# Optimization experiments

Measured on AMD Instinct MI355X. Metric: run time of the kernel, lower is better.

## Reference

```python
import jax, jax.numpy as jnp
import numpy as np

N_NODES = 2048
N_PAIRS = 65536
D = 512
P = 16


def setup_inputs() -> dict:
    key = jax.random.key(0)
    ks = jax.random.split(key, 9)
    scale = 1.0 / np.sqrt(D)
    obj_feats = jax.random.normal(ks[0], (N_NODES, D), dtype=jnp.float32)
    union_feats = jax.random.normal(ks[1], (N_PAIRS, D), dtype=jnp.float32)
    pair_idxs = jax.random.randint(ks[2], (N_PAIRS, 2), 0, N_NODES, dtype=jnp.int64)
    ws_w = jax.random.uniform(ks[3], (D, D), jnp.float32, -scale, scale)
    ws_b = jax.random.uniform(ks[4], (D,), jnp.float32, -scale, scale)
    wo_w = jax.random.uniform(ks[5], (D, D), jnp.float32, -scale, scale)
    wo_b = jax.random.uniform(ks[6], (D,), jnp.float32, -scale, scale)
    w_w = jax.random.uniform(ks[7], (P, D), jnp.float32, -scale, scale)
    w_b = jax.random.uniform(ks[8], (P,), jnp.float32, -scale, scale)
    return {
        'obj_feats': obj_feats, 'union_feats': union_feats, 'pair_idxs': pair_idxs,
        'ws_w': ws_w, 'ws_b': ws_b, 'wo_w': wo_w, 'wo_b': wo_b, 'w_w': w_w, 'w_b': w_b,
    }


def reference(obj_feats, union_feats, pair_idxs, ws_w, ws_b, wo_w, wo_b, w_w, w_b):
    n = obj_feats.shape[0]
    p = w_w.shape[0]
    # node projections: [N, D]
    s = obj_feats @ ws_w.T + ws_b
    o = obj_feats @ wo_w.T + wo_b
    # gather pair features and fuse elementwise product: [E, D]
    prod = s[pair_idxs[:, 0]] * o[pair_idxs[:, 1]] * union_feats
    # project to p attention logits per pair: [E, p]
    atten_f = prod @ w_w.T + w_b
    # scatter into dense [N, N, p]
    atten = jnp.zeros((n, n, p), dtype=obj_feats.dtype)
    atten = atten.at[pair_idxs[:, 0], pair_idxs[:, 1]].add(atten_f)
    # mask diagonal with -1e4 and softmax over axis=1 (incoming nodes)
    atten = atten - jnp.eye(n, dtype=obj_feats.dtype)[:, :, None] * 10000.0
    return jax.nn.softmax(atten, axis=1)
```

## Files before the change

kernel.cpp:

```cpp
#include <hip/hip_runtime.h>
#include <hip/hip_bf16.h>

#define N_NODES 2048
#define N_PAIRS 65536
#define DIM 512
#define NP 16
#define SLOTS 96
#define SP 520

typedef __attribute__((ext_vector_type(8))) short s16x8;
typedef __attribute__((ext_vector_type(8))) unsigned short u16x8;
typedef __attribute__((ext_vector_type(4))) float f32x4;

static __device__ __forceinline__ unsigned short f2bf(float x) {
    union { float f; unsigned int u; } v; v.f = x;
    unsigned int r = v.u + 0x7FFFu + ((v.u >> 16) & 1u);
    return (unsigned short)(r >> 16);
}
static __device__ __forceinline__ float bf2f(unsigned short u) {
    union { unsigned int u; float f; } v; v.u = ((unsigned int)u) << 16;
    return v.f;
}
static __device__ __forceinline__ u16x8 pack8(float4 a, float4 b) {
    u16x8 r;
    r[0]=f2bf(a.x); r[1]=f2bf(a.y); r[2]=f2bf(a.z); r[3]=f2bf(a.w);
    r[4]=f2bf(b.x); r[5]=f2bf(b.y); r[6]=f2bf(b.z); r[7]=f2bf(b.w);
    return r;
}

#define GBM 64
#define GBN 64
#define GBK 32
#define GSA 40

__global__ __launch_bounds__(256) void gemm_so(
    const float* __restrict__ A, const float* __restrict__ Ws, const float* __restrict__ bsv,
    const float* __restrict__ Wo, const float* __restrict__ bov,
    unsigned short* __restrict__ Sb, unsigned short* __restrict__ Ob)
{
    __shared__ unsigned short As[GBM*GSA];
    __shared__ unsigned short Bs[GBN*GSA];
    const int tid = threadIdx.x;
    const int m0 = blockIdx.y*GBM, n0 = blockIdx.x*GBN;
    const int ar = tid>>2, ac = (tid&3)*8;
    const float* Arow = A + (size_t)(m0+ar)*DIM + ac;
    const int nrow = n0 + ar;
    const float* Wrow = (nrow < DIM ? Ws + (size_t)nrow*DIM : Wo + (size_t)(nrow-DIM)*DIM) + ac;
    float4 a_r[2], b_r[2];
    a_r[0] = *(const float4*)(Arow);   a_r[1] = *(const float4*)(Arow+4);
    b_r[0] = *(const float4*)(Wrow);   b_r[1] = *(const float4*)(Wrow+4);

    const int lane = tid&63, wid = tid>>6;
    const int wm = (wid>>1)*32, wn = (wid&1)*32;
    const int fr = lane&15, ks8 = (lane>>4)*8;
    f32x4 acc[2][2] = {};
    for (int k0=0; k0<DIM; k0+=GBK) {
        *(u16x8*)&As[ar*GSA+ac] = pack8(a_r[0],a_r[1]);
        *(u16x8*)&Bs[ar*GSA+ac] = pack8(b_r[0],b_r[1]);
        __syncthreads();
        if (k0+GBK < DIM) {
            a_r[0] = *(const float4*)(Arow + k0+GBK);   a_r[1] = *(const float4*)(Arow + k0+GBK + 4);
            b_r[0] = *(const float4*)(Wrow + k0+GBK);   b_r[1] = *(const float4*)(Wrow + k0+GBK + 4);
        }
        s16x8 af[2], bfr[2];
        #pragma unroll
        for (int mi=0;mi<2;++mi) af[mi]  = *(const s16x8*)&As[(wm+mi*16+fr)*GSA + ks8];
        #pragma unroll
        for (int ni=0;ni<2;++ni) bfr[ni] = *(const s16x8*)&Bs[(wn+ni*16+fr)*GSA + ks8];
        #pragma unroll
        for (int mi=0;mi<2;++mi)
            #pragma unroll
            for (int ni=0;ni<2;++ni)
                acc[mi][ni] = __builtin_amdgcn_mfma_f32_16x16x32_bf16(af[mi], bfr[ni], acc[mi][ni], 0,0,0);
        __syncthreads();
    }
    const int rg = lane>>4;
    #pragma unroll
    for (int ni=0;ni<2;++ni) {
        const int n = n0 + wn + ni*16 + fr;
        const float bias = (n < DIM) ? bsv[n] : bov[n-DIM];
        unsigned short* dst = (n < DIM) ? (Sb + n) : (Ob + (n - DIM));
        #pragma unroll
        for (int mi=0;mi<2;++mi) {
            #pragma unroll
            for (int q=0;q<4;++q) {
                const int m = m0 + wm + mi*16 + rg*4 + q;
                dst[(size_t)m*DIM] = f2bf(acc[mi][ni][q] + bias);
            }
        }
    }
}

__global__ __launch_bounds__(256) void pairproj_k(
    const unsigned short* __restrict__ Sb, const unsigned short* __restrict__ Ob,
    const float* __restrict__ U, const int* __restrict__ idx,
    const float* __restrict__ w_w, const float* __restrict__ w_b,
    int* __restrict__ rowcnt, int* __restrict__ rowj, float* __restrict__ rowv)
{
    __shared__ unsigned short P[4*8*SP];
    const int tid = threadIdx.x;
    const int lane = tid&63, wid = tid>>6;
    const int fr = lane&15, ks8 = (lane>>4)*8;
    s16x8 wreg[16];
    #pragma unroll
    for (int st=0;st<16;++st) {
        const float4* wp = (const float4*)(w_w + (size_t)fr*DIM + st*32 + ks8);
        u16x8 t = pack8(wp[0], wp[1]);
        wreg[st] = *(s16x8*)&t;
    }
    const float wbv = w_b[fr];
    unsigned short* Pw = &P[wid*8*SP];
    const int eb = blockIdx.x*128 + wid*32;
    for (int it=0; it<4; ++it) {
        const int e0 = eb + it*8;
        #pragma unroll 4
        for (int s8=0; s8<8; ++s8) {
            const int e = e0 + s8;
            const int i = idx[2*e], j = idx[2*e+1];
            u16x8 sv = *(const u16x8*)(Sb + (size_t)i*DIM + lane*8);
            u16x8 ov = *(const u16x8*)(Ob + (size_t)j*DIM + lane*8);
            const float4* up = (const float4*)(U + (size_t)e*DIM + lane*8);
            float4 u0 = up[0], u1 = up[1];
            float4 p0, p1;
            p0.x = bf2f(sv[0])*bf2f(ov[0])*u0.x;
            p0.y = bf2f(sv[1])*bf2f(ov[1])*u0.y;
            p0.z = bf2f(sv[2])*bf2f(ov[2])*u0.z;
            p0.w = bf2f(sv[3])*bf2f(ov[3])*u0.w;
            p1.x = bf2f(sv[4])*bf2f(ov[4])*u1.x;
            p1.y = bf2f(sv[5])*bf2f(ov[5])*u1.y;
            p1.z = bf2f(sv[6])*bf2f(ov[6])*u1.z;
            p1.w = bf2f(sv[7])*bf2f(ov[7])*u1.w;
            *(u16x8*)&Pw[s8*SP + lane*8] = pack8(p0, p1);
        }
        f32x4 acc = {0.f,0.f,0.f,0.f};
        #pragma unroll
        for (int st=0;st<16;++st) {
            s16x8 af = *(const s16x8*)&Pw[(fr&7)*SP + st*32 + ks8];
            acc = __builtin_amdgcn_mfma_f32_16x16x32_bf16(af, wreg[st], acc, 0,0,0);
        }
        int iv = 0, posv = 0;
        if (lane < 8) {
            const int e = e0 + lane;
            iv = idx[2*e];
            const int jv = idx[2*e + 1];
            posv = atomicAdd(&rowcnt[iv], 1);
            if (posv < SLOTS) rowj[iv*SLOTS + posv] = jv;
        }
        const int rg = lane>>4;
        #pragma unroll
        for (int q=0;q<4;++q) {
            const int pr = rg*4 + q;
            if (pr < 8) {
                const int ip = __shfl(iv, pr, 64);
                const int pp = __shfl(posv, pr, 64);
                if (pp < SLOTS)
                    rowv[((size_t)ip*SLOTS + pp)*NP + fr] = acc[q] + wbv;
            }
        }
    }
}

__global__ __launch_bounds__(256) void softmax_k(
    const int* __restrict__ rowcnt, const int* __restrict__ rowj,
    const float* __restrict__ rowv, float* __restrict__ out)
{
    __shared__ __align__(16) float vals[SLOTS][NP];
    __shared__ int jcol[SLOTS];
    __shared__ unsigned char dead[SLOTS];
    __shared__ float red[16][17];
    __shared__ float mP[NP], invZ[NP], bg[NP];
    __shared__ int ndistinct;
    const int i = blockIdx.x;
    const int t = threadIdx.x;
    int c = rowcnt[i];
    if (c > SLOTS) c = SLOTS;

    if (t == 0) ndistinct = 0;
    for (int a = t; a < c; a += 256) {
        jcol[a] = rowj[i*SLOTS + a];
        dead[a] = 0;
        const float4* src = (const float4*)(rowv + ((size_t)i*SLOTS + a)*NP);
        float4* dst = (float4*)vals[a];
        dst[0] = src[0]; dst[1] = src[1]; dst[2] = src[2]; dst[3] = src[3];
    }
    __syncthreads();

    for (int a = t; a < c; a += 256) {
        int j = jcol[a];
        int first = a;
        for (int b = 0; b < a; ++b) if (jcol[b] == j) { first = b; break; }
        if (first != a) {
            dead[a] = 1;
            #pragma unroll
            for (int p = 0; p < NP; ++p) atomicAdd(&vals[first][p], vals[a][p]);
        }
    }
    __syncthreads();
    for (int a = t; a < c; a += 256)
        if (!dead[a] && jcol[a] != i) atomicAdd(&ndistinct, 1);
    __syncthreads();

    const int p = t & 15, ch = t >> 4;
    float pm = 0.f;
    for (int a = ch; a < c; a += 16)
        if (!dead[a] && jcol[a] != i) pm = fmaxf(pm, vals[a][p]);
    red[ch][p] = pm;
    __syncthreads();
    if (t < NP) {
        float m = 0.f;
        #pragma unroll
        for (int k = 0; k < 16; ++k) m = fmaxf(m, red[k][t]);
        mP[t] = m;
    }
    __syncthreads();
    {
        const float m = mP[p];
        float ps = 0.f;
        for (int a = ch; a < c; a += 16)
            if (!dead[a] && jcol[a] != i) ps += __expf(vals[a][p] - m);
        red[ch][p] = ps;
    }
    __syncthreads();
    if (t < NP) {
        float zs = 0.f;
        #pragma unroll
        for (int k = 0; k < 16; ++k) zs += red[k][t];
        const float m = mP[t];
        const float eb = __expf(-m);
        const float nbg = (float)(N_NODES - 1 - ndistinct);
        const float Z = zs + nbg * eb;
        const float iz = 1.0f / Z;
        invZ[t] = iz; bg[t] = eb * iz;
    }
    __syncthreads();

    const size_t rowbase = (size_t)i * N_NODES * NP;
    {
        const int g = t & 3;
        float4 b4 = make_float4(bg[g*4+0], bg[g*4+1], bg[g*4+2], bg[g*4+3]);
        float4* orow = (float4*)(out + rowbase);
        #pragma unroll 8
        for (int n = 0; n < 32; ++n) orow[t + 256 * n] = b4;
    }
    __syncthreads();

    for (int a = t; a < c; a += 256) {
        if (dead[a]) continue;
        const int j = jcol[a];
        float4* dst = (float4*)(out + rowbase + (size_t)j * NP);
        if (j == i) {
            float4 z = make_float4(0.f, 0.f, 0.f, 0.f);
            dst[0] = z; dst[1] = z; dst[2] = z; dst[3] = z;
        } else {
            #pragma unroll
            for (int q = 0; q < 4; ++q) {
                float4 v;
                v.x = __expf(vals[a][4*q+0] - mP[4*q+0]) * invZ[4*q+0];
                v.y = __expf(vals[a][4*q+1] - mP[4*q+1]) * invZ[4*q+1];
                v.z = __expf(vals[a][4*q+2] - mP[4*q+2]) * invZ[4*q+2];
                v.w = __expf(vals[a][4*q+3] - mP[4*q+3]) * invZ[4*q+3];
                dst[q] = v;
            }
        }
    }
    if (t == 0) {
        float4 z = make_float4(0.f, 0.f, 0.f, 0.f);
        float4* dst = (float4*)(out + rowbase + (size_t)i * NP);
        dst[0] = z; dst[1] = z; dst[2] = z; dst[3] = z;
    }
}

extern "C" void kernel_launch(void* const* d_in, const int* in_sizes, int n_in,
                              void* d_out, int out_size, void* d_ws, size_t ws_size,
                              hipStream_t stream)
{
    (void)in_sizes; (void)n_in; (void)out_size; (void)ws_size;
    const float* obj  = (const float*)d_in[0];
    const float* uni  = (const float*)d_in[1];
    const int*   idx  = (const int*)  d_in[2];
    const float* ws_w = (const float*)d_in[3];
    const float* ws_b = (const float*)d_in[4];
    const float* wo_w = (const float*)d_in[5];
    const float* wo_b = (const float*)d_in[6];
    const float* w_w  = (const float*)d_in[7];
    const float* w_b  = (const float*)d_in[8];
    float* out = (float*)d_out;

    unsigned short* Sb = (unsigned short*)d_ws;
    unsigned short* Ob = Sb + (size_t)N_NODES * DIM;
    float* rowv  = (float*)(Ob + (size_t)N_NODES * DIM);
    int* rowj    = (int*)(rowv + (size_t)N_NODES * SLOTS * NP);
    int* rowcnt  = rowj + (size_t)N_NODES * SLOTS;

    hipMemsetAsync(rowcnt, 0, N_NODES * sizeof(int), stream);
    gemm_so<<<dim3(1024/GBN, N_NODES/GBM), 256, 0, stream>>>(obj, ws_w, ws_b, wo_w, wo_b, Sb, Ob);
    pairproj_k<<<N_PAIRS/128, 256, 0, stream>>>(Sb, Ob, uni, idx, w_w, w_b, rowcnt, rowj, rowv);
    softmax_k<<<N_NODES, 256, 0, stream>>>(rowcnt, rowj, rowv, out);
}
```

Before: 138.2 us.

## Fuse rowcnt zeroing into GEMM, fill full MFMA tile, use nontemporal output stores

Removes the separate memset launch by having the first 8 GEMM blocks zero the per-row counters. The pair-projection kernel now processes 16 pairs per MFMA tile instead of 8, so all 16 rows of the 16x16 tile carry useful work and the number of MFMA passes is halved. The softmax kernel writes its large dense output with nontemporal stores to avoid polluting the cache. Together these cut launch overhead and wasted MFMA work, and the output write is the dominant memory traffic.

```diff
diff --git a/kernel.cpp b/kernel.cpp
--- a/kernel.cpp
+++ b/kernel.cpp
@@ -27,6 +27,10 @@
     r[4]=f2bf(b.x); r[5]=f2bf(b.y); r[6]=f2bf(b.z); r[7]=f2bf(b.w);
     return r;
 }
+static __device__ __forceinline__ void store_nt4(float* p, float a, float b, float c, float d) {
+    f32x4 v = {a, b, c, d};
+    __builtin_nontemporal_store(v, (f32x4*)p);
+}
 
 #define GBM 64
 #define GBN 64
@@ -36,11 +40,16 @@
 __global__ __launch_bounds__(256) void gemm_so(
     const float* __restrict__ A, const float* __restrict__ Ws, const float* __restrict__ bsv,
     const float* __restrict__ Wo, const float* __restrict__ bov,
-    unsigned short* __restrict__ Sb, unsigned short* __restrict__ Ob)
+    unsigned short* __restrict__ Sb, unsigned short* __restrict__ Ob,
+    int* __restrict__ rowcnt)
 {
     __shared__ unsigned short As[GBM*GSA];
     __shared__ unsigned short Bs[GBN*GSA];
     const int tid = threadIdx.x;
+    {
+        const int bid = blockIdx.y * gridDim.x + blockIdx.x;
+        if (bid < 8) rowcnt[bid*256 + tid] = 0;
+    }
     const int m0 = blockIdx.y*GBM, n0 = blockIdx.x*GBN;
     const int ar = tid>>2, ac = (tid&3)*8;
     const float* Arow = A + (size_t)(m0+ar)*DIM + ac;
@@ -97,7 +106,7 @@
     const float* __restrict__ w_w, const float* __restrict__ w_b,
     int* __restrict__ rowcnt, int* __restrict__ rowj, float* __restrict__ rowv)
 {
-    __shared__ unsigned short P[4*8*SP];
+    __shared__ unsigned short P[4*16*SP];
     const int tid = threadIdx.x;
     const int lane = tid&63, wid = tid>>6;
     const int fr = lane&15, ks8 = (lane>>4)*8;
@@ -109,12 +118,12 @@
         wreg[st] = *(s16x8*)&t;
     }
     const float wbv = w_b[fr];
-    unsigned short* Pw = &P[wid*8*SP];
+    unsigned short* Pw = &P[wid*16*SP];
     const int eb = blockIdx.x*128 + wid*32;
-    for (int it=0; it<4; ++it) {
-        const int e0 = eb + it*8;
+    for (int it=0; it<2; ++it) {
+        const int e0 = eb + it*16;
         #pragma unroll 4
-        for (int s8=0; s8<8; ++s8) {
+        for (int s8=0; s8<16; ++s8) {
             const int e = e0 + s8;
             const int i = idx[2*e], j = idx[2*e+1];
             u16x8 sv = *(const u16x8*)(Sb + (size_t)i*DIM + lane*8);
@@ -135,11 +144,11 @@
         f32x4 acc = {0.f,0.f,0.f,0.f};
         #pragma unroll
         for (int st=0;st<16;++st) {
-            s16x8 af = *(const s16x8*)&Pw[(fr&7)*SP + st*32 + ks8];
+            s16x8 af = *(const s16x8*)&Pw[fr*SP + st*32 + ks8];
             acc = __builtin_amdgcn_mfma_f32_16x16x32_bf16(af, wreg[st], acc, 0,0,0);
         }
         int iv = 0, posv = 0;
-        if (lane < 8) {
+        if (lane < 16) {
             const int e = e0 + lane;
             iv = idx[2*e];
             const int jv = idx[2*e + 1];
@@ -150,12 +159,10 @@
         #pragma unroll
         for (int q=0;q<4;++q) {
             const int pr = rg*4 + q;
-            if (pr < 8) {
-                const int ip = __shfl(iv, pr, 64);
-                const int pp = __shfl(posv, pr, 64);
-                if (pp < SLOTS)
-                    rowv[((size_t)ip*SLOTS + pp)*NP + fr] = acc[q] + wbv;
-            }
+            const int ip = __shfl(iv, pr, 64);
+            const int pp = __shfl(posv, pr, 64);
+            if (pp < SLOTS)
+                rowv[((size_t)ip*SLOTS + pp)*NP + fr] = acc[q] + wbv;
         }
     }
 }
@@ -237,36 +244,40 @@
     const size_t rowbase = (size_t)i * N_NODES * NP;
     {
         const int g = t & 3;
-        float4 b4 = make_float4(bg[g*4+0], bg[g*4+1], bg[g*4+2], bg[g*4+3]);
-        float4* orow = (float4*)(out + rowbase);
+        const float b0 = bg[g*4+0], b1 = bg[g*4+1], b2 = bg[g*4+2], b3 = bg[g*4+3];
+        float* orow = out + rowbase;
         #pragma unroll 8
-        for (int n = 0; n < 32; ++n) orow[t + 256 * n] = b4;
+        for (int n = 0; n < 32; ++n)
+            store_nt4(orow + 4*(t + 256*n), b0, b1, b2, b3);
     }
     __syncthreads();
 
     for (int a = t; a < c; a += 256) {
         if (dead[a]) continue;
         const int j = jcol[a];
-        float4* dst = (float4*)(out + rowbase + (size_t)j * NP);
+        float* dst = out + rowbase + (size_t)j * NP;
         if (j == i) {
-            float4 z = make_float4(0.f, 0.f, 0.f, 0.f);
-            dst[0] = z; dst[1] = z; dst[2] = z; dst[3] = z;
+            store_nt4(dst+0,  0.f,0.f,0.f,0.f);
+            store_nt4(dst+4,  0.f,0.f,0.f,0.f);
+            store_nt4(dst+8,  0.f,0.f,0.f,0.f);
+            store_nt4(dst+12, 0.f,0.f,0.f,0.f);
         } else {
             #pragma unroll
             for (int q = 0; q < 4; ++q) {
-                float4 v;
-                v.x = __expf(vals[a][4*q+0] - mP[4*q+0]) * invZ[4*q+0];
-                v.y = __expf(vals[a][4*q+1] - mP[4*q+1]) * invZ[4*q+1];
-                v.z = __expf(vals[a][4*q+2] - mP[4*q+2]) * invZ[4*q+2];
-                v.w = __expf(vals[a][4*q+3] - mP[4*q+3]) * invZ[4*q+3];
-                dst[q] = v;
+                store_nt4(dst + 4*q,
+                    __expf(vals[a][4*q+0] - mP[4*q+0]) * invZ[4*q+0],
+                    __expf(vals[a][4*q+1] - mP[4*q+1]) * invZ[4*q+1],
+                    __expf(vals[a][4*q+2] - mP[4*q+2]) * invZ[4*q+2],
+                    __expf(vals[a][4*q+3] - mP[4*q+3]) * invZ[4*q+3]);
             }
         }
     }
     if (t == 0) {
-        float4 z = make_float4(0.f, 0.f, 0.f, 0.f);
-        float4* dst = (float4*)(out + rowbase + (size_t)i * NP);
-        dst[0] = z; dst[1] = z; dst[2] = z; dst[3] = z;
+        float* dst = out + rowbase + (size_t)i * NP;
+        store_nt4(dst+0,  0.f,0.f,0.f,0.f);
+        store_nt4(dst+4,  0.f,0.f,0.f,0.f);
+        store_nt4(dst+8,  0.f,0.f,0.f,0.f);
+        store_nt4(dst+12, 0.f,0.f,0.f,0.f);
     }
 }
 
@@ -292,8 +303,7 @@
     int* rowj    = (int*)(rowv + (size_t)N_NODES * SLOTS * NP);
     int* rowcnt  = rowj + (size_t)N_NODES * SLOTS;
 
-    hipMemsetAsync(rowcnt, 0, N_NODES * sizeof(int), stream);
-    gemm_so<<<dim3(1024/GBN, N_NODES/GBM), 256, 0, stream>>>(obj, ws_w, ws_b, wo_w, wo_b, Sb, Ob);
+    gemm_so<<<dim3(1024/GBN, N_NODES/GBM), 256, 0, stream>>>(obj, ws_w, ws_b, wo_w, wo_b, Sb, Ob, rowcnt);
     pairproj_k<<<N_PAIRS/128, 256, 0, stream>>>(Sb, Ob, uni, idx, w_w, w_b, rowcnt, rowj, rowv);
     softmax_k<<<N_NODES, 256, 0, stream>>>(rowcnt, rowj, rowv, out);
 }
```

After: 122.8 us, median of 2. 11.1% less time.
